# Kernel tuning notes

Measured on AMD Instinct MI355X. Metric: run time of the kernel, lower is better.

Reference implementation:

```python
import jax, jax.numpy as jnp
import numpy as np
from jax import lax

IOU_THRESHOLD = 0.1
B, N = 4, 8192


def setup_inputs() -> dict:
    key = jax.random.key(0)
    # [B, 5, N]: rows 0..3 = cx, cy, w, h; row 4 = confidence score in (0, 1)
    outputs = jax.random.uniform(key, (B, 5, N), dtype=jnp.float32)
    return {"outputs": outputs}


def _nms_single(p):
    """Greedy NMS on one image. p: [5, N] -> [5, N] with kept boxes
    compacted to the front (original column order preserved) and the rest
    zero-padded. Matches the torch loop: repeatedly take the highest-scoring
    surviving box, drop all boxes with IoU >= threshold (box keeps itself),
    and drop boxes with score <= 0."""
    boxes, scores = p[:4], p[4]
    n = scores.shape[0]
    order = jnp.argsort(-scores)            # descending score order
    b = boxes[:, order]

    x1 = b[0] - b[2] * 0.5
    y1 = b[1] - b[3] * 0.5
    x2 = b[0] + b[2] * 0.5
    y2 = b[1] + b[3] * 0.5
    area = (x2 - x1) * (y2 - y1)

    iw = jnp.clip(jnp.minimum(x2[:, None], x2[None, :]) - jnp.maximum(x1[:, None], x1[None, :]), 0.0)
    ih = jnp.clip(jnp.minimum(y2[:, None], y2[None, :]) - jnp.maximum(y1[:, None], y1[None, :]), 0.0)
    inter = iw * ih
    union = area[:, None] + area[None, :] - inter
    iou = inter / (union + 1e-8)            # [N, N] in sorted order

    idx_range = jnp.arange(n)
    keep_init = scores[order] > 0           # non_zero_scores filter

    def body(i, keep):
        # if box i (in score order) survives, suppress j with IoU >= thr, j != i
        row_keep = (iou[i] < IOU_THRESHOLD) | (idx_range == i)
        return jnp.where(keep[i], keep & row_keep, keep)

    keep_sorted = lax.fori_loop(0, n, body, keep_init)

    # map keep mask back to original column order
    keep_orig = jnp.zeros((n,), bool).at[order].set(keep_sorted)
    # stable compaction: kept columns first, original relative order preserved
    perm = jnp.argsort(jnp.where(keep_orig, 0, 1), stable=True)
    gathered = p[:, perm]                    # [5, N]
    valid = idx_range < jnp.sum(keep_orig)
    return jnp.where(valid[None, :], gathered, 0.0)


def reference(outputs):
    # torch version pads to the max detections across the batch; here we keep
    # the fixed width N (extra columns are zero), same kept values/order.
    return jax.vmap(_nms_single)(outputs)


if __name__ == "__main__":
    inp = setup_inputs()
    out = jax.jit(reference)(**inp)
    print(out.shape, out.dtype)
```

## Files before the change

kernel.cpp:

```cpp
#include <hip/hip_runtime.h>

#pragma clang fp contract(off)

#define NBOX 8192
#define BLK  1024
#define EPT  8
#define NBUCK 2048
#define NB 256
#define IOU_THR 0.1f

typedef unsigned short u16;
typedef unsigned int u32;
typedef unsigned long long u64;

#define MND 0x1.999999p-4

#define SMEM_TOT 161408

__global__ __launch_bounds__(BLK, 4) void nms_kernel(const float* __restrict__ in,
                                                     float* __restrict__ out) {
    __shared__ __align__(16) char smem[SMEM_TOT];
    const int img = blockIdx.x;
    const float* __restrict__ p = in + (size_t)img * 5 * NBOX;
    float* __restrict__ o = out + (size_t)img * 5 * NBOX;
    const int t = threadIdx.x;
    const int lane = t & 63;
    const int wid = t >> 6;

    float4* box   = (float4*)smem;
    u16* A        = (u16*)(smem + 131072);
    float4* bx    = (float4*)(smem + 147456);
    u64 (*mat)[4] = (u64(*)[4])(smem + 151552);
    float4* kx    = (float4*)(smem + 155648);
    u32* pfxA     = (u32*)(smem + 151552);
    u32* kom      = (u32*)(smem + 159744);
    int* wcnt     = (int*)(smem + 160768);
    u64* keptQ    = (u64*)(smem + 160832);
    int* S0sh     = (int*)(smem + 160864);
    u64* skey  = (u64*)smem;
    u32* hist  = (u32*)(smem + 65536);
    u32* bbase = (u32*)(smem + 73728);

    {
        float4 z; z.x = z.y = z.z = z.w = 0.0f;
        float4* o4 = (float4*)o;
#pragma unroll
        for (int e = 0; e < 10; e++) o4[t + e * BLK] = z;
    }

    for (int i = t; i < NBUCK; i += BLK) hist[i] = 0;
    if (t < 256) kom[t] = 0;
    if (t == 0) *S0sh = 0;
    __syncthreads();

    u32 mybkt[EPT], myarr[EPT], mykeyhi[EPT];
#pragma unroll
    for (int e = 0; e < EPT; e++) {
        int j = t + e * BLK;
        float s = p[4 * NBOX + j];
        u32 u = __float_as_uint(s);
        u32 ordb = u ^ (u32)(((int)u >> 31) | (int)0x80000000);
        mykeyhi[e] = ~ordb;
        int vb = (int)(s * (float)NBUCK);
        vb = vb < 0 ? 0 : (vb > NBUCK - 1 ? NBUCK - 1 : vb);
        mybkt[e] = (u32)(NBUCK - 1 - vb);
        myarr[e] = atomicAdd(&hist[mybkt[e]], 1u);
        u64 bal = __ballot(s > 0.0f);
        if (lane == 0) atomicAdd(S0sh, (int)__popcll(bal));
    }
    __syncthreads();

    {
        u32 h0 = hist[2 * t], h1 = hist[2 * t + 1];
        int v = (int)(h0 + h1);
        int x = v;
        for (int d = 1; d < 64; d <<= 1) {
            int y = __shfl_up(x, d, 64);
            if (lane >= d) x += y;
        }
        if (lane == 63) wcnt[wid] = x;
        __syncthreads();
        int wb = 0;
        for (int i = 0; i < wid; i++) wb += wcnt[i];
        int excl = wb + x - v;
        bbase[2 * t] = (u32)excl;
        bbase[2 * t + 1] = (u32)excl + h0;
    }
    __syncthreads();

#pragma unroll
    for (int e = 0; e < EPT; e++) {
        u32 pos = bbase[mybkt[e]] + myarr[e];
        skey[pos] = ((u64)mykeyhi[e] << 32) | (u32)(t + e * BLK);
    }
    __syncthreads();

#pragma unroll
    for (int e = 0; e < EPT; e++) {
        u32 b = mybkt[e];
        u32 lo = bbase[b], hi2 = lo + hist[b];
        u64 me = ((u64)mykeyhi[e] << 32) | (u32)(t + e * BLK);
        u32 r = lo;
        for (u32 q = lo; q < hi2; q++) r += (skey[q] < me) ? 1u : 0u;
        A[r] = (u16)(t + e * BLK);
    }
    __syncthreads();
    int S = *S0sh;

#pragma unroll
    for (int e = 0; e < EPT; e++) {
        int j = t + e * BLK;
        float cx = p[j], cy = p[NBOX + j];
        float w_ = p[2 * NBOX + j], h_ = p[3 * NBOX + j];
        box[j] = make_float4(cx - w_ * 0.5f, cy - h_ * 0.5f,
                             cx + w_ * 0.5f, cy + h_ * 0.5f);
    }
    __syncthreads();

    if (t < NB) bx[t] = box[A[t]];
    ((u64*)mat)[t] = 0;
    __syncthreads();

    while (S > 0) {
        int nb = S < NB ? S : NB;

        {
            int i = t >> 2, q = t & 3;
            if (i > 0 && i < nb) {
                int clo = (i * q) >> 2;
                int chi = (i * (q + 1)) >> 2;
                if (chi > clo) {
                    float4 bi = bx[i];
                    float ari = (bi.z - bi.x) * (bi.w - bi.y);
                    u64 acc = 0;
                    for (int c = clo; c < chi; c++) {
                        float4 bc = bx[c];
                        float arc = (bc.z - bc.x) * (bc.w - bc.y);
                        float iw = fmaxf(fminf(bi.z, bc.z) - fmaxf(bi.x, bc.x), 0.0f);
                        float ih = fmaxf(fminf(bi.w, bc.w) - fmaxf(bi.y, bc.y), 0.0f);
                        float inter = iw * ih;
                        float t2 = (ari + arc) - inter;
                        float uu = t2 + 1e-8f;
                        if ((double)inter > MND * (double)uu) acc |= (1ull << (c - clo));
                    }
                    if (acc) {
                        int w0 = clo >> 6, sh = clo & 63;
                        atomicOr(&mat[i][w0], acc << sh);
                        if (sh && (((chi - 1) >> 6) != w0))
                            atomicOr(&mat[i][w0 + 1], acc >> (64 - sh));
                    }
                }
            }
        }
        __syncthreads();

        int tailN = S - nb;
        int C1 = 0, base0 = nb;
        if (tailN > 0) {
            int lim = tailN < 7680 ? tailN : 7680;
            C1 = (lim + 959) / 960;
            base0 = nb + 960 * C1;
        }
        float4 eb[EPT]; float ea[EPT]; u16 ei[EPT];
        u32 am = 0;
        if (wid == 0) {
            u64 r0[4], r1[4], r2[4], r3[4];
#pragma unroll
            for (int wq = 0; wq < 4; wq++) {
                r0[wq] = mat[lane][wq];
                r1[wq] = mat[64 + lane][wq];
                r2[wq] = mat[128 + lane][wq];
                r3[wq] = mat[192 + lane][wq];
            }
            u64 A0, A1, A2, A3;
            {
                int n0 = nb;       A0 = n0 <= 0 ? 0ull : (n0 >= 64 ? ~0ull : ((1ull << n0) - 1ull));
                int n1 = nb - 64;  A1 = n1 <= 0 ? 0ull : (n1 >= 64 ? ~0ull : ((1ull << n1) - 1ull));
                int n2 = nb - 128; A2 = n2 <= 0 ? 0ull : (n2 >= 64 ? ~0ull : ((1ull << n2) - 1ull));
                int n3 = nb - 192; A3 = n3 <= 0 ? 0ull : (n3 >= 64 ? ~0ull : ((1ull << n3) - 1ull));
            }
            u64 K0 = 0, K1 = 0, K2 = 0, K3 = 0;
            u64 lm = (1ull << lane) - 1ull;
            while (A0 | A1 | A2 | A3) {
                bool c0b = ((A0 >> lane) & 1) && !(r0[0] & A0 & lm);
                bool c1b = ((A1 >> lane) & 1) && !((r1[0] & A0) | (r1[1] & A1 & lm));
                bool c2b = ((A2 >> lane) & 1) && !((r2[0] & A0) | (r2[1] & A1) | (r2[2] & A2 & lm));
                bool c3b = ((A3 >> lane) & 1) && !((r3[0] & A0) | (r3[1] & A1) | (r3[2] & A2) | (r3[3] & A3 & lm));
                u64 C0_ = __ballot(c0b), C1_ = __ballot(c1b), C2_ = __ballot(c2b), C3_ = __ballot(c3b);
                K0 |= C0_; K1 |= C1_; K2 |= C2_; K3 |= C3_;
                A0 &= ~C0_; A1 &= ~C1_; A2 &= ~C2_; A3 &= ~C3_;
                bool s0b = ((A0 >> lane) & 1) && ((r0[0] & C0_) | (r0[1] & C1_) | (r0[2] & C2_) | (r0[3] & C3_));
                bool s1b = ((A1 >> lane) & 1) && ((r1[0] & C0_) | (r1[1] & C1_) | (r1[2] & C2_) | (r1[3] & C3_));
                bool s2b = ((A2 >> lane) & 1) && ((r2[0] & C0_) | (r2[1] & C1_) | (r2[2] & C2_) | (r2[3] & C3_));
                bool s3b = ((A3 >> lane) & 1) && ((r3[0] & C0_) | (r3[1] & C1_) | (r3[2] & C2_) | (r3[3] & C3_));
                A0 &= ~__ballot(s0b); A1 &= ~__ballot(s1b); A2 &= ~__ballot(s2b); A3 &= ~__ballot(s3b);
            }
            if (lane < 4) keptQ[lane] = lane == 0 ? K0 : lane == 1 ? K1 : lane == 2 ? K2 : K3;
        } else {
            int ti = t - 64;
            int st = nb + ti * C1;
#pragma unroll
            for (int e = 0; e < EPT; e++) {
                int pos = st + e;
                if (e < C1 && pos < S) {
                    u16 j = A[pos];
                    ei[e] = j;
                    float4 b = box[j];
                    eb[e] = b;
                    ea[e] = (b.z - b.x) * (b.w - b.y);
                    am |= (1u << e);
                }
            }
        }
        __syncthreads();

        if (t < 512) ((u64*)mat)[t] = 0;
        u64 kq0 = keptQ[0], kq1 = keptQ[1], kq2 = keptQ[2], kq3 = keptQ[3];
        int nk = (int)(__popcll(kq0) + __popcll(kq1) + __popcll(kq2) + __popcll(kq3));
        if (t < nb) {
            int wq = t >> 6;
            u64 kq = wq == 0 ? kq0 : wq == 1 ? kq1 : wq == 2 ? kq2 : kq3;
            if ((kq >> (t & 63)) & 1) {
                int j = (int)A[t];
                atomicOr(&kom[j >> 5], 1u << (j & 31));
                int pk = 0;
                if (wq > 0) pk += (int)__popcll(kq0);
                if (wq > 1) pk += (int)__popcll(kq1);
                if (wq > 2) pk += (int)__popcll(kq2);
                pk += (int)__popcll(kq & ((1ull << (t & 63)) - 1ull));
                kx[pk] = bx[t];
            }
        }
        if (wid == 0 && base0 < S) {
            int C0 = (S - base0 + 63) >> 6;
            int st0 = base0 + lane * C0;
#pragma unroll
            for (int e = 0; e < EPT; e++) {
                int pos = st0 + e;
                if (e < C0 && pos < S) {
                    u16 j = A[pos];
                    ei[e] = j;
                    float4 b = box[j];
                    eb[e] = b;
                    ea[e] = (b.z - b.x) * (b.w - b.y);
                    am |= (1u << e);
                }
            }
        }
        __syncthreads();

        if (am) {
            for (int c = 0; c < nk; c++) {
                float4 cb = kx[c];
                float arc = (cb.z - cb.x) * (cb.w - cb.y);
#pragma unroll
                for (int e = 0; e < EPT; e++) {
                    if (am & (1u << e)) {
                        float iw = fminf(eb[e].z, cb.z) - fmaxf(eb[e].x, cb.x);
                        float ih = fminf(eb[e].w, cb.w) - fmaxf(eb[e].y, cb.y);
                        if (iw > 0.0f && ih > 0.0f) {
                            float inter = iw * ih;
                            float t2 = (ea[e] + arc) - inter;
                            float uu = t2 + 1e-8f;
                            if ((double)inter > MND * (double)uu) am &= ~(1u << e);
                        }
                    }
                }
                if (!am) break;
            }
        }

        {
            int cnt = __popc(am);
            int x = cnt;
            for (int d = 1; d < 64; d <<= 1) {
                int y = __shfl_up(x, d, 64);
                if (lane >= d) x += y;
            }
            if (lane == 63) wcnt[wid] = x;
            __syncthreads();
            int wb = 0, tot = 0;
            for (int i = 0; i < 16; i++) tot += wcnt[i];
            if (wid == 0) {
                for (int i = 1; i < 16; i++) wb += wcnt[i];
            } else {
                for (int i = 1; i < wid; i++) wb += wcnt[i];
            }
            int off = wb + x - cnt;
#pragma unroll
            for (int e = 0; e < EPT; e++) {
                if (am & (1u << e)) {
                    A[off] = ei[e];
                    if (off < NB) bx[off] = eb[e];
                    off++;
                }
            }
            if (t >= 512) ((u64*)mat)[t] = 0;
            __syncthreads();
            S = tot;
        }
    }
    __syncthreads();

    {
        u32 w = (t < 256) ? kom[t] : 0u;
        int c = __popc(w);
        int x = c;
        for (int d = 1; d < 64; d <<= 1) {
            int y = __shfl_up(x, d, 64);
            if (lane >= d) x += y;
        }
        if (lane == 63) wcnt[wid] = x;
        __syncthreads();
        int wb = 0;
        for (int i = 0; i < wid; i++) wb += wcnt[i];
        if (t < 256) pfxA[t] = (u32)(wb + x - c);
    }
    __syncthreads();
    for (int j = t; j < NBOX; j += BLK) {
        u32 km = kom[j >> 5];
        if ((km >> (j & 31)) & 1u) {
            int pos = (int)(pfxA[j >> 5] + (u32)__popc(km & ((1u << (j & 31)) - 1u)));
            o[0 * NBOX + pos] = p[0 * NBOX + j];
            o[1 * NBOX + pos] = p[1 * NBOX + j];
            o[2 * NBOX + pos] = p[2 * NBOX + j];
            o[3 * NBOX + pos] = p[3 * NBOX + j];
            o[4 * NBOX + pos] = p[4 * NBOX + j];
        }
    }
}

extern "C" void kernel_launch(void* const* d_in, const int* in_sizes, int n_in,
                              void* d_out, int out_size, void* d_ws, size_t ws_size,
                              hipStream_t stream) {
    const float* in = (const float*)d_in[0];
    float* out = (float*)d_out;
    int B = in_sizes[0] / (5 * NBOX);
    hipLaunchKernelGGL(nms_kernel, dim3(B), dim3(BLK), 0, stream, in, out);
}
```

Baseline: 153.6 us.

## Double score buckets and move kept-box scatter into wave 0 to drop a barrier

Doubles the number of histogram buckets used for the bucketed score sort, so each bucket holds fewer keys and the in-bucket rank loop runs shorter. The prefix scan now handles four buckets per thread. It also moves the kept-box compaction (kom bitmask, kx scatter) and wave 0's next-chunk load into wave 0 itself, right after the greedy resolve. That removes one __syncthreads per iteration of the block loop. The risk is that the serial work now sits on one wave while other waves may read kx and kom without a barrier.

```diff
diff --git a/kernel.cpp b/kernel.cpp
--- a/kernel.cpp
+++ b/kernel.cpp
@@ -5,7 +5,7 @@
 #define NBOX 8192
 #define BLK  1024
 #define EPT  8
-#define NBUCK 2048
+#define NBUCK 4096
 #define NB 256
 #define IOU_THR 0.1f
 
@@ -39,7 +39,7 @@
     int* S0sh     = (int*)(smem + 160864);
     u64* skey  = (u64*)smem;
     u32* hist  = (u32*)(smem + 65536);
-    u32* bbase = (u32*)(smem + 73728);
+    u32* bbase = (u32*)(smem + 81920);
 
     {
         float4 z; z.x = z.y = z.z = z.w = 0.0f;
@@ -71,8 +71,8 @@
     __syncthreads();
 
     {
-        u32 h0 = hist[2 * t], h1 = hist[2 * t + 1];
-        int v = (int)(h0 + h1);
+        u32 h0 = hist[4 * t], h1 = hist[4 * t + 1], h2 = hist[4 * t + 2], h3 = hist[4 * t + 3];
+        int v = (int)(h0 + h1 + h2 + h3);
         int x = v;
         for (int d = 1; d < 64; d <<= 1) {
             int y = __shfl_up(x, d, 64);
@@ -83,8 +83,10 @@
         int wb = 0;
         for (int i = 0; i < wid; i++) wb += wcnt[i];
         int excl = wb + x - v;
-        bbase[2 * t] = (u32)excl;
-        bbase[2 * t + 1] = (u32)excl + h0;
+        bbase[4 * t]     = (u32)excl;
+        bbase[4 * t + 1] = (u32)excl + h0;
+        bbase[4 * t + 2] = (u32)excl + h0 + h1;
+        bbase[4 * t + 3] = (u32)excl + h0 + h1 + h2;
     }
     __syncthreads();
 
@@ -196,6 +198,39 @@
                 A0 &= ~__ballot(s0b); A1 &= ~__ballot(s1b); A2 &= ~__ballot(s2b); A3 &= ~__ballot(s3b);
             }
             if (lane < 4) keptQ[lane] = lane == 0 ? K0 : lane == 1 ? K1 : lane == 2 ? K2 : K3;
+            {
+                int pkb1 = (int)__popcll(K0);
+                int pkb2 = pkb1 + (int)__popcll(K1);
+                int pkb3 = pkb2 + (int)__popcll(K2);
+#pragma unroll
+                for (int wq = 0; wq < 4; wq++) {
+                    u64 kq = wq == 0 ? K0 : wq == 1 ? K1 : wq == 2 ? K2 : K3;
+                    if ((kq >> lane) & 1) {
+                        int slot = wq * 64 + lane;
+                        int j = (int)A[slot];
+                        atomicOr(&kom[j >> 5], 1u << (j & 31));
+                        int pk = (wq == 0 ? 0 : wq == 1 ? pkb1 : wq == 2 ? pkb2 : pkb3)
+                                 + (int)__popcll(kq & lm);
+                        kx[pk] = bx[slot];
+                    }
+                }
+            }
+            if (base0 < S) {
+                int C0 = (S - base0 + 63) >> 6;
+                int st0 = base0 + lane * C0;
+#pragma unroll
+                for (int e = 0; e < EPT; e++) {
+                    int pos = st0 + e;
+                    if (e < C0 && pos < S) {
+                        u16 j = A[pos];
+                        ei[e] = j;
+                        float4 b = box[j];
+                        eb[e] = b;
+                        ea[e] = (b.z - b.x) * (b.w - b.y);
+                        am |= (1u << e);
+                    }
+                }
+            }
         } else {
             int ti = t - 64;
             int st = nb + ti * C1;
@@ -217,37 +252,6 @@
         if (t < 512) ((u64*)mat)[t] = 0;
         u64 kq0 = keptQ[0], kq1 = keptQ[1], kq2 = keptQ[2], kq3 = keptQ[3];
         int nk = (int)(__popcll(kq0) + __popcll(kq1) + __popcll(kq2) + __popcll(kq3));
-        if (t < nb) {
-            int wq = t >> 6;
-            u64 kq = wq == 0 ? kq0 : wq == 1 ? kq1 : wq == 2 ? kq2 : kq3;
-            if ((kq >> (t & 63)) & 1) {
-                int j = (int)A[t];
-                atomicOr(&kom[j >> 5], 1u << (j & 31));
-                int pk = 0;
-                if (wq > 0) pk += (int)__popcll(kq0);
-                if (wq > 1) pk += (int)__popcll(kq1);
-                if (wq > 2) pk += (int)__popcll(kq2);
-                pk += (int)__popcll(kq & ((1ull << (t & 63)) - 1ull));
-                kx[pk] = bx[t];
-            }
-        }
-        if (wid == 0 && base0 < S) {
-            int C0 = (S - base0 + 63) >> 6;
-            int st0 = base0 + lane * C0;
-#pragma unroll
-            for (int e = 0; e < EPT; e++) {
-                int pos = st0 + e;
-                if (e < C0 && pos < S) {
-                    u16 j = A[pos];
-                    ei[e] = j;
-                    float4 b = box[j];
-                    eb[e] = b;
-                    ea[e] = (b.z - b.x) * (b.w - b.y);
-                    am |= (1u << e);
-                }
-            }
-        }
-        __syncthreads();
 
         if (am) {
             for (int c = 0; c < nk; c++) {
```

Result: no change. 152.2 us (median of 2 runs) (-0.9%).
